# Optimization experiments

Hardware: AMD Instinct MI355X
Metric: run time of the kernel (lower is better)

The kernel has to match this reference:

```python
import jax, jax.numpy as jnp
import numpy as np

B, V = 256, 128000


def setup_inputs() -> dict:
    key = jax.random.key(0)
    k1, k2 = jax.random.split(key)
    logits = jax.random.normal(k1, (B, V), dtype=jnp.float32) * 4.0
    # temperatures in [0.3, 1.2] to avoid division by ~0
    temperatures = jax.random.uniform(k2, (B,), dtype=jnp.float32) * 0.9 + 0.3
    return {"logits": logits, "temperatures": temperatures}


def reference(logits, temperatures):
    # temperature-scaled softmax
    x = logits.astype(jnp.float32) / temperatures[:, None]
    probs = jax.nn.softmax(x, axis=-1)  # (B, V)
    # torch.empty_like(probs).exponential_(1).clamp_min_(1e-10)
    noise = jnp.maximum(
        jax.random.exponential(jax.random.key(42), probs.shape, dtype=jnp.float32),
        1e-10,
    )
    # Gumbel-max style sampling: argmax of probs / Exp(1) noise
    return jnp.argmax(probs / noise, axis=-1)  # (B,) int
```

## Files before the change

### kernel.cpp

```cpp
#include <hip/hip_runtime.h>
#include <stdint.h>
#include <math.h>

#define BB 256
#define ROW 128000
#define SPLIT 16
#define CHUNK (ROW / SPLIT)
#define THREADS 512
#define WAVES (THREADS / 64)
#define EPB (THREADS * 8)
#define GRID (BB * SPLIT)
#define CAP 6144

#define SEED_THREADS 256
#define SEED_STRIDE 496

#define TF_K2 0x1BD11BF0u
#define SMALL_BITS 0x00100000u
#define MIN_L 1.4426950408889634e-10f
#define LN2 0.69314718055994530942f
#define GMAX 33.0f

__device__ __forceinline__ uint32_t rotl32(uint32_t x, int r) {
    return __builtin_amdgcn_alignbit(x, x, 32 - r);
}

#define R1S(r)        { x0 += x1; x1 = rotl32(x1, (r)) ^ x0; }
#define RI1S(r, A, B) { x1 += (B); x0 = x0 + (A) + x1; x1 = rotl32(x1, (r)) ^ x0; }

__device__ __forceinline__ uint32_t threefry1_xor(uint32_t c) {
    uint32_t x1 = c + 42u;
    uint32_t x0 = x1;
    x1 = rotl32(x1, 13) ^ x0;
    R1S(15) R1S(26) R1S(6)
    RI1S(17, 42u, TF_K2 + 1u)
    R1S(29) R1S(16) R1S(24)
    RI1S(13, TF_K2, 2u)
    R1S(15) R1S(26) R1S(6)
    RI1S(17, 0u, 45u)
    R1S(29) R1S(16) R1S(24)
    RI1S(13, 42u, TF_K2 + 4u)
    R1S(15) R1S(26) R1S(6)
    return (x0 + TF_K2) ^ (x1 + 5u);
}

__device__ __forceinline__ void threefry8_xor(uint32_t c, uint32_t bits[8]) {
    uint32_t x0[8], x1[8];
#pragma unroll
    for (int j = 0; j < 8; ++j) x1[j] = c + (uint32_t)(j + 42);
#pragma unroll
    for (int j = 0; j < 8; ++j) { x0[j] = x1[j]; x1[j] = rotl32(x1[j], 13) ^ x0[j]; }

#define RND(r)                                        \
    do { _Pragma("unroll")                            \
        for (int j = 0; j < 8; ++j) {                 \
            x0[j] += x1[j];                           \
            x1[j] = rotl32(x1[j], (r)) ^ x0[j];       \
        } } while (0)
#define RNDI(r, A, B)                                 \
    do { _Pragma("unroll")                            \
        for (int j = 0; j < 8; ++j) {                 \
            x1[j] += (B);                             \
            x0[j] = x0[j] + (A) + x1[j];              \
            x1[j] = rotl32(x1[j], (r)) ^ x0[j];       \
        } } while (0)

    RND(15); RND(26); RND(6);
    RNDI(17, 42u, TF_K2 + 1u);
    RND(29); RND(16); RND(24);
    RNDI(13, TF_K2, 2u);
    RND(15); RND(26); RND(6);
    RNDI(17, 0u, 45u);
    RND(29); RND(16); RND(24);
    RNDI(13, 42u, TF_K2 + 4u);
    RND(15); RND(26); RND(6);
#undef RND
#undef RNDI

#pragma unroll
    for (int j = 0; j < 8; ++j) bits[j] = (x0[j] + TF_K2) ^ (x1[j] + 5u);
}

__device__ __forceinline__ float noise_negL(uint32_t bits) {
    const float uf = __uint_as_float(0x3F800000u | (bits >> 9));
    const float L = __builtin_amdgcn_logf(2.0f - uf);
    const float u = uf - 1.0f;
    const float es2 = u * fmaf(u, fmaf(u, fmaf(u,
        -0.3606737602222408f, -0.4808983469629878f),
        -0.7213475204444817f), -1.4426950408889634f);
    const float es2c = fminf(es2, -MIN_L);
    return (bits < SMALL_BITS) ? es2c : L;
}

__device__ __forceinline__ float score1(float x, float invT2, uint32_t bits) {
    const float L = noise_negL(bits);
    return fmaf(x, invT2, -__builtin_amdgcn_logf(-L));
}

__device__ __forceinline__ uint32_t f2o(float f) {
    uint32_t u = __float_as_uint(f);
    return (u & 0x80000000u) ? ~u : (u | 0x80000000u);
}

__global__ __launch_bounds__(SEED_THREADS) void seed_kernel(
    const float* __restrict__ logits,
    const float* __restrict__ temps,
    float* __restrict__ gs) {
    const int b = blockIdx.x;
    const int t = threadIdx.x;
    const float invT2 = 1.0f / (temps[b] * LN2);
    const int off = t * SEED_STRIDE;
    const float* rowp = logits + (size_t)b * ROW + off;
    const uint32_t cb = (uint32_t)b * ROW + (uint32_t)off;

    const float4 xa = *reinterpret_cast<const float4*>(rowp);
    const float4 xb = *reinterpret_cast<const float4*>(rowp + 4);
    const float xs[8] = {xa.x, xa.y, xa.z, xa.w, xb.x, xb.y, xb.z, xb.w};
    uint32_t bits[8];
    threefry8_xor(cb, bits);

    float bs = -INFINITY;
#pragma unroll
    for (int j = 0; j < 8; ++j) bs = fmaxf(bs, score1(xs[j], invT2, bits[j]));

#pragma unroll
    for (int off2 = 32; off2 >= 1; off2 >>= 1)
        bs = fmaxf(bs, __shfl_xor(bs, off2));

    __shared__ float sred[SEED_THREADS / 64];
    const int lane = t & 63, wid = t >> 6;
    if (lane == 0) sred[wid] = bs;
    __syncthreads();
    if (t == 0)
        gs[b] = fmaxf(fmaxf(sred[0], sred[1]), fmaxf(sred[2], sred[3]));
}

__global__ __launch_bounds__(THREADS, 4) void sampler_kernel(
    const float* __restrict__ logits,
    const float* __restrict__ temps,
    const float* __restrict__ gs,
    unsigned long long* __restrict__ parts) {
    __shared__ int scnt;
    __shared__ unsigned short qidx[CAP];
    __shared__ float qx[CAP];
    __shared__ unsigned long long sbest[WAVES];

    const int g = blockIdx.x;
    const int b = g >> 4;
    const int q = g & 15;
    const float T = temps[b];
    const float invT2 = 1.0f / (T * LN2);
    const float xthr = (gs[b] - GMAX) * (T * LN2);
    const float* rowp = logits + (size_t)b * ROW + (size_t)q * CHUNK;
    const uint32_t cbase = (uint32_t)b * ROW + (uint32_t)(q * CHUNK);
    const int tid = threadIdx.x;
    const int lane = tid & 63;
    const unsigned long long lmask_lt = (1ull << lane) - 1ull;

    if (tid == 0) scnt = 0;
    __syncthreads();

    float xs0[8], xs1[8];
    {
        const int rel = tid * 8;
        const float4 xa = *reinterpret_cast<const float4*>(rowp + rel);
        const float4 xb = *reinterpret_cast<const float4*>(rowp + rel + 4);
        xs0[0]=xa.x; xs0[1]=xa.y; xs0[2]=xa.z; xs0[3]=xa.w;
        xs0[4]=xb.x; xs0[5]=xb.y; xs0[6]=xb.z; xs0[7]=xb.w;
#pragma unroll
        for (int j = 0; j < 8; ++j) {
            const bool pass = xs0[j] > xthr;
            const unsigned long long mk = __ballot(pass);
            if (mk != 0ull) {
                int base = 0;
                if (lane == 0) base = atomicAdd(&scnt, __popcll(mk));
                base = __builtin_amdgcn_readfirstlane(base);
                if (pass) {
                    const int pos = base + (int)__popcll(mk & lmask_lt);
                    if (pos < CAP) {
                        qidx[pos] = (unsigned short)(rel + j);
                        qx[pos] = xs0[j];
                    }
                }
            }
        }
    }
    const int rel1 = EPB + tid * 8;
    const bool in1 = rel1 < CHUNK;
    if (in1) {
        const float4 xa = *reinterpret_cast<const float4*>(rowp + rel1);
        const float4 xb = *reinterpret_cast<const float4*>(rowp + rel1 + 4);
        xs1[0]=xa.x; xs1[1]=xa.y; xs1[2]=xa.z; xs1[3]=xa.w;
        xs1[4]=xb.x; xs1[5]=xb.y; xs1[6]=xb.z; xs1[7]=xb.w;
#pragma unroll
        for (int j = 0; j < 8; ++j) {
            const bool pass = xs1[j] > xthr;
            const unsigned long long mk = __ballot(pass);
            if (mk != 0ull) {
                int base = 0;
                if (lane == 0) base = atomicAdd(&scnt, __popcll(mk));
                base = __builtin_amdgcn_readfirstlane(base);
                if (pass) {
                    const int pos = base + (int)__popcll(mk & lmask_lt);
                    if (pos < CAP) {
                        qidx[pos] = (unsigned short)(rel1 + j);
                        qx[pos] = xs1[j];
                    }
                }
            }
        }
    }
    __syncthreads();

    const int total = scnt;
    float best_s = -INFINITY;
    uint32_t best_rel = 0u;

    if (total > CAP) {
        {
            const int rel = tid * 8;
            uint32_t bits[8];
            threefry8_xor(cbase + (uint32_t)rel, bits);
#pragma unroll
            for (int j = 0; j < 8; ++j) {
                const float s = score1(xs0[j], invT2, bits[j]);
                if (s > best_s) { best_s = s; best_rel = (uint32_t)(rel + j); }
            }
        }
        if (in1) {
            uint32_t bits[8];
            threefry8_xor(cbase + (uint32_t)rel1, bits);
#pragma unroll
            for (int j = 0; j < 8; ++j) {
                const float s = score1(xs1[j], invT2, bits[j]);
                if (s > best_s) { best_s = s; best_rel = (uint32_t)(rel1 + j); }
            }
        }
    } else {
        for (int i = tid; i < total; i += THREADS) {
            const int rel = (int)qidx[i];
            const float x = qx[i];
            const uint32_t bits = threefry1_xor(cbase + (uint32_t)rel);
            const float s = score1(x, invT2, bits);
            if (s > best_s) { best_s = s; best_rel = (uint32_t)rel; }
        }
    }

    const uint32_t best_v = (uint32_t)(q * CHUNK) + best_rel;

    unsigned long long best =
        ((unsigned long long)f2o(best_s) << 32) | (uint32_t)(~best_v);
#pragma unroll
    for (int off = 32; off >= 1; off >>= 1) {
        const unsigned long long o = __shfl_xor(best, off);
        best = (o > best) ? o : best;
    }
    const int wid = tid >> 6;
    if (lane == 0) sbest[wid] = best;
    __syncthreads();
    if (tid == 0) {
        unsigned long long r = sbest[0];
#pragma unroll
        for (int w = 1; w < WAVES; ++w) r = (sbest[w] > r) ? sbest[w] : r;
        parts[g] = r;
    }
}

__global__ __launch_bounds__(BB) void combine_kernel(
    const unsigned long long* __restrict__ parts, int* __restrict__ out) {
    const int b = threadIdx.x;
    const unsigned long long* p = parts + b * SPLIT;
    unsigned long long r = p[0];
#pragma unroll
    for (int w = 1; w < SPLIT; ++w) r = (p[w] > r) ? p[w] : r;
    out[b] = (int)(~(uint32_t)(r & 0xFFFFFFFFull));
}

extern "C" void kernel_launch(void* const* d_in, const int* in_sizes, int n_in,
                              void* d_out, int out_size, void* d_ws, size_t ws_size,
                              hipStream_t stream) {
    const float* logits = (const float*)d_in[0];
    const float* temps = (const float*)d_in[1];
    int* out = (int*)d_out;
    float* gs = (float*)d_ws;
    unsigned long long* parts = (unsigned long long*)((char*)d_ws + 1024);

    hipLaunchKernelGGL(seed_kernel, dim3(BB), dim3(SEED_THREADS), 0, stream,
                       logits, temps, gs);
    hipLaunchKernelGGL(sampler_kernel, dim3(GRID), dim3(THREADS), 0, stream,
                       logits, temps, gs, parts);
    hipLaunchKernelGGL(combine_kernel, dim3(1), dim3(BB), 0, stream, parts, out);
}
```

Measured before the change: 88.48 us.

## Add chunk-max prepass to tighten pruning threshold and pick per-row dense/sparse mode

Adds a chunkmax kernel that reads the whole logits array to find each 4000-element chunk's max logit. The seed kernel folds the noise scores at those maxima into the row bound and counts how many samples pass the threshold, so it can choose a dense or sparse mode per row. The sampler now uses 32 chunks per row and stores only indices in shared memory, re-reading x from global memory. In dense mode it skips the small-value polynomial unless some lane needs it. The cost is one extra full pass over the 131 MB input and an extra kernel launch.

```diff
diff --git a/kernel.cpp b/kernel.cpp
--- a/kernel.cpp
+++ b/kernel.cpp
@@ -4,13 +4,11 @@
 
 #define BB 256
 #define ROW 128000
-#define SPLIT 16
-#define CHUNK (ROW / SPLIT)
+#define SPLITM 32
+#define CHUNKM (ROW / SPLITM)
+#define GRIDM (BB * SPLITM)
 #define THREADS 512
 #define WAVES (THREADS / 64)
-#define EPB (THREADS * 8)
-#define GRID (BB * SPLIT)
-#define CAP 6144
 
 #define SEED_THREADS 256
 #define SEED_STRIDE 496
@@ -20,6 +18,7 @@
 #define MIN_L 1.4426950408889634e-10f
 #define LN2 0.69314718055994530942f
 #define GMAX 33.0f
+#define MODE_CNT_THR 1152
 
 __device__ __forceinline__ uint32_t rotl32(uint32_t x, int r) {
     return __builtin_amdgcn_alignbit(x, x, 32 - r);
@@ -102,13 +101,54 @@
     return (u & 0x80000000u) ? ~u : (u | 0x80000000u);
 }
 
-__global__ __launch_bounds__(SEED_THREADS) void seed_kernel(
-    const float* __restrict__ logits,
-    const float* __restrict__ temps,
-    float* __restrict__ gs) {
+__global__ __launch_bounds__(THREADS) void chunkmax_kernel(
+    const float* __restrict__ logits, float* __restrict__ cmx,
+    uint32_t* __restrict__ cmi) {
+    const int g = blockIdx.x;
+    const int b = g >> 5, q = g & 31;
+    const float* rowp = logits + (size_t)b * ROW + (size_t)q * CHUNKM;
+    const int tid = threadIdx.x;
+    const int rel = tid * 8;
+
+    float mx = -INFINITY;
+    uint32_t mi = 0u;
+    if (rel < CHUNKM) {
+        const float4 xa = *reinterpret_cast<const float4*>(rowp + rel);
+        const float4 xb = *reinterpret_cast<const float4*>(rowp + rel + 4);
+        const float xs[8] = {xa.x, xa.y, xa.z, xa.w, xb.x, xb.y, xb.z, xb.w};
+#pragma unroll
+        for (int j = 0; j < 8; ++j)
+            if (xs[j] > mx) { mx = xs[j]; mi = (uint32_t)(rel + j); }
+    }
+#pragma unroll
+    for (int off = 32; off >= 1; off >>= 1) {
+        const float ox = __shfl_xor(mx, off);
+        const uint32_t oi = __shfl_xor(mi, off);
+        if (ox > mx) { mx = ox; mi = oi; }
+    }
+    __shared__ float smx[WAVES];
+    __shared__ uint32_t smi[WAVES];
+    const int lane = tid & 63, wid = tid >> 6;
+    if (lane == 0) { smx[wid] = mx; smi[wid] = mi; }
+    __syncthreads();
+    if (tid == 0) {
+        mx = smx[0]; mi = smi[0];
+#pragma unroll
+        for (int w = 1; w < WAVES; ++w)
+            if (smx[w] > mx) { mx = smx[w]; mi = smi[w]; }
+        cmx[g] = mx;
+        cmi[g] = (uint32_t)(q * CHUNKM) + mi;
+    }
+}
+
+__global__ __launch_bounds__(SEED_THREADS) void rowseed_kernel(
+    const float* __restrict__ logits, const float* __restrict__ temps,
+    const float* __restrict__ cmx, const uint32_t* __restrict__ cmi,
+    float* __restrict__ gs, int* __restrict__ mode) {
     const int b = blockIdx.x;
     const int t = threadIdx.x;
-    const float invT2 = 1.0f / (temps[b] * LN2);
+    const float T = temps[b];
+    const float invT2 = 1.0f / (T * LN2);
     const int off = t * SEED_STRIDE;
     const float* rowp = logits + (size_t)b * ROW + off;
     const uint32_t cb = (uint32_t)b * ROW + (uint32_t)off;
@@ -123,36 +163,52 @@
 #pragma unroll
     for (int j = 0; j < 8; ++j) bs = fmaxf(bs, score1(xs[j], invT2, bits[j]));
 
-#pragma unroll
-    for (int off2 = 32; off2 >= 1; off2 >>= 1)
-        bs = fmaxf(bs, __shfl_xor(bs, off2));
-
+    if (t < SPLITM) {
+        const uint32_t idx = cmi[b * SPLITM + t];
+        const float xm = cmx[b * SPLITM + t];
+        bs = fmaxf(bs, score1(xm, invT2,
+                              threefry1_xor((uint32_t)b * ROW + idx)));
+    }
+
+#pragma unroll
+    for (int o = 32; o >= 1; o >>= 1) bs = fmaxf(bs, __shfl_xor(bs, o));
     __shared__ float sred[SEED_THREADS / 64];
+    __shared__ int scr[SEED_THREADS / 64];
     const int lane = t & 63, wid = t >> 6;
     if (lane == 0) sred[wid] = bs;
     __syncthreads();
-    if (t == 0)
-        gs[b] = fmaxf(fmaxf(sred[0], sred[1]), fmaxf(sred[2], sred[3]));
+    const float gsv = fmaxf(fmaxf(sred[0], sred[1]), fmaxf(sred[2], sred[3]));
+
+    const float xthr = (gsv - GMAX) * (T * LN2);
+    int c = 0;
+#pragma unroll
+    for (int j = 0; j < 8; ++j) c += (xs[j] > xthr) ? 1 : 0;
+#pragma unroll
+    for (int o = 32; o >= 1; o >>= 1) c += __shfl_xor(c, o);
+    if (lane == 0) scr[wid] = c;
+    __syncthreads();
+    if (t == 0) {
+        const int tot = scr[0] + scr[1] + scr[2] + scr[3];
+        gs[b] = gsv;
+        mode[b] = (tot > MODE_CNT_THR) ? 1 : 0;
+    }
 }
 
 __global__ __launch_bounds__(THREADS, 4) void sampler_kernel(
-    const float* __restrict__ logits,
-    const float* __restrict__ temps,
-    const float* __restrict__ gs,
+    const float* __restrict__ logits, const float* __restrict__ temps,
+    const float* __restrict__ gs, const int* __restrict__ mode,
     unsigned long long* __restrict__ parts) {
     __shared__ int scnt;
-    __shared__ unsigned short qidx[CAP];
-    __shared__ float qx[CAP];
+    __shared__ unsigned short qidx[CHUNKM];
     __shared__ unsigned long long sbest[WAVES];
 
     const int g = blockIdx.x;
-    const int b = g >> 4;
-    const int q = g & 15;
+    const int b = g >> 5, q = g & 31;
     const float T = temps[b];
     const float invT2 = 1.0f / (T * LN2);
     const float xthr = (gs[b] - GMAX) * (T * LN2);
-    const float* rowp = logits + (size_t)b * ROW + (size_t)q * CHUNK;
-    const uint32_t cbase = (uint32_t)b * ROW + (uint32_t)(q * CHUNK);
+    const float* rowp = logits + (size_t)b * ROW + (size_t)q * CHUNKM;
+    const uint32_t cbase = (uint32_t)b * ROW + (uint32_t)(q * CHUNKM);
     const int tid = threadIdx.x;
     const int lane = tid & 63;
     const unsigned long long lmask_lt = (1ull << lane) - 1ull;
@@ -160,94 +216,79 @@
     if (tid == 0) scnt = 0;
     __syncthreads();
 
-    float xs0[8], xs1[8];
-    {
-        const int rel = tid * 8;
+    const int rel = tid * 8;
+    const bool act = rel < CHUNKM;
+    float xs[8];
+    if (act) {
         const float4 xa = *reinterpret_cast<const float4*>(rowp + rel);
         const float4 xb = *reinterpret_cast<const float4*>(rowp + rel + 4);
-        xs0[0]=xa.x; xs0[1]=xa.y; xs0[2]=xa.z; xs0[3]=xa.w;
-        xs0[4]=xb.x; xs0[5]=xb.y; xs0[6]=xb.z; xs0[7]=xb.w;
-#pragma unroll
-        for (int j = 0; j < 8; ++j) {
-            const bool pass = xs0[j] > xthr;
-            const unsigned long long mk = __ballot(pass);
-            if (mk != 0ull) {
-                int base = 0;
-                if (lane == 0) base = atomicAdd(&scnt, __popcll(mk));
-                base = __builtin_amdgcn_readfirstlane(base);
-                if (pass) {
-                    const int pos = base + (int)__popcll(mk & lmask_lt);
-                    if (pos < CAP) {
+        xs[0]=xa.x; xs[1]=xa.y; xs[2]=xa.z; xs[3]=xa.w;
+        xs[4]=xb.x; xs[5]=xb.y; xs[6]=xb.z; xs[7]=xb.w;
+    }
+
+    float best_s = -INFINITY;
+    uint32_t best_rel = 0u;
+
+    if (mode[b]) {
+        if (act) {
+            uint32_t bits[8];
+            threefry8_xor(cbase + (uint32_t)rel, bits);
+            float L8[8];
+#pragma unroll
+            for (int j = 0; j < 8; ++j) {
+                const float uf = __uint_as_float(0x3F800000u | (bits[j] >> 9));
+                L8[j] = __builtin_amdgcn_logf(2.0f - uf);
+            }
+            const uint32_t b01 = min(min(bits[0], bits[1]), bits[2]);
+            const uint32_t b34 = min(min(bits[3], bits[4]), bits[5]);
+            const uint32_t b67 = min(bits[6], bits[7]);
+            if (__any(min(min(b01, b34), b67) < SMALL_BITS)) {
+#pragma unroll
+                for (int j = 0; j < 8; ++j) {
+                    const float u = __uint_as_float(0x3F800000u |
+                                    (bits[j] >> 9)) - 1.0f;
+                    const float es2 = u * fmaf(u, fmaf(u, fmaf(u,
+                        -0.3606737602222408f, -0.4808983469629878f),
+                        -0.7213475204444817f), -1.4426950408889634f);
+                    const float es2c = fminf(es2, -MIN_L);
+                    L8[j] = (bits[j] < SMALL_BITS) ? es2c : L8[j];
+                }
+            }
+#pragma unroll
+            for (int j = 0; j < 8; ++j) {
+                const float s = fmaf(xs[j], invT2,
+                                     -__builtin_amdgcn_logf(-L8[j]));
+                if (s > best_s) { best_s = s; best_rel = (uint32_t)(rel + j); }
+            }
+        }
+    } else {
+        if (act) {
+#pragma unroll
+            for (int j = 0; j < 8; ++j) {
+                const bool pass = xs[j] > xthr;
+                const unsigned long long mk = __ballot(pass);
+                if (mk != 0ull) {
+                    int base = 0;
+                    if (lane == 0) base = atomicAdd(&scnt, __popcll(mk));
+                    base = __builtin_amdgcn_readfirstlane(base);
+                    if (pass) {
+                        const int pos = base + (int)__popcll(mk & lmask_lt);
                         qidx[pos] = (unsigned short)(rel + j);
-                        qx[pos] = xs0[j];
                     }
                 }
             }
         }
-    }
-    const int rel1 = EPB + tid * 8;
-    const bool in1 = rel1 < CHUNK;
-    if (in1) {
-        const float4 xa = *reinterpret_cast<const float4*>(rowp + rel1);
-        const float4 xb = *reinterpret_cast<const float4*>(rowp + rel1 + 4);
-        xs1[0]=xa.x; xs1[1]=xa.y; xs1[2]=xa.z; xs1[3]=xa.w;
-        xs1[4]=xb.x; xs1[5]=xb.y; xs1[6]=xb.z; xs1[7]=xb.w;
-#pragma unroll
-        for (int j = 0; j < 8; ++j) {
-            const bool pass = xs1[j] > xthr;
-            const unsigned long long mk = __ballot(pass);
-            if (mk != 0ull) {
-                int base = 0;
-                if (lane == 0) base = atomicAdd(&scnt, __popcll(mk));
-                base = __builtin_amdgcn_readfirstlane(base);
-                if (pass) {
-                    const int pos = base + (int)__popcll(mk & lmask_lt);
-                    if (pos < CAP) {
-                        qidx[pos] = (unsigned short)(rel1 + j);
-                        qx[pos] = xs1[j];
-                    }
-                }
-            }
+        __syncthreads();
+        const int total = scnt;
+        for (int i = tid; i < total; i += THREADS) {
+            const int r2 = (int)qidx[i];
+            const float x = rowp[r2];
+            const float s = score1(x, invT2, threefry1_xor(cbase + (uint32_t)r2));
+            if (s > best_s) { best_s = s; best_rel = (uint32_t)r2; }
         }
     }
-    __syncthreads();
-
-    const int total = scnt;
-    float best_s = -INFINITY;
-    uint32_t best_rel = 0u;
-
-    if (total > CAP) {
-        {
-            const int rel = tid * 8;
-            uint32_t bits[8];
-            threefry8_xor(cbase + (uint32_t)rel, bits);
-#pragma unroll
-            for (int j = 0; j < 8; ++j) {
-                const float s = score1(xs0[j], invT2, bits[j]);
-                if (s > best_s) { best_s = s; best_rel = (uint32_t)(rel + j); }
-            }
-        }
-        if (in1) {
-            uint32_t bits[8];
-            threefry8_xor(cbase + (uint32_t)rel1, bits);
-#pragma unroll
-            for (int j = 0; j < 8; ++j) {
-                const float s = score1(xs1[j], invT2, bits[j]);
-                if (s > best_s) { best_s = s; best_rel = (uint32_t)(rel1 + j); }
-            }
-        }
-    } else {
-        for (int i = tid; i < total; i += THREADS) {
-            const int rel = (int)qidx[i];
-            const float x = qx[i];
-            const uint32_t bits = threefry1_xor(cbase + (uint32_t)rel);
-            const float s = score1(x, invT2, bits);
-            if (s > best_s) { best_s = s; best_rel = (uint32_t)rel; }
-        }
-    }
-
-    const uint32_t best_v = (uint32_t)(q * CHUNK) + best_rel;
-
+
+    const uint32_t best_v = (uint32_t)(q * CHUNKM) + best_rel;
     unsigned long long best =
         ((unsigned long long)f2o(best_s) << 32) | (uint32_t)(~best_v);
 #pragma unroll
@@ -269,10 +310,10 @@
 __global__ __launch_bounds__(BB) void combine_kernel(
     const unsigned long long* __restrict__ parts, int* __restrict__ out) {
     const int b = threadIdx.x;
-    const unsigned long long* p = parts + b * SPLIT;
+    const unsigned long long* p = parts + b * SPLITM;
     unsigned long long r = p[0];
 #pragma unroll
-    for (int w = 1; w < SPLIT; ++w) r = (p[w] > r) ? p[w] : r;
+    for (int w = 1; w < SPLITM; ++w) r = (p[w] > r) ? p[w] : r;
     out[b] = (int)(~(uint32_t)(r & 0xFFFFFFFFull));
 }
 
@@ -282,12 +323,18 @@
     const float* logits = (const float*)d_in[0];
     const float* temps = (const float*)d_in[1];
     int* out = (int*)d_out;
-    float* gs = (float*)d_ws;
-    unsigned long long* parts = (unsigned long long*)((char*)d_ws + 1024);
-
-    hipLaunchKernelGGL(seed_kernel, dim3(BB), dim3(SEED_THREADS), 0, stream,
-                       logits, temps, gs);
-    hipLaunchKernelGGL(sampler_kernel, dim3(GRID), dim3(THREADS), 0, stream,
-                       logits, temps, gs, parts);
+    float* cmx = (float*)d_ws;
+    uint32_t* cmi = (uint32_t*)((char*)d_ws + 32768);
+    float* gs = (float*)((char*)d_ws + 65536);
+    int* mode = (int*)((char*)d_ws + 66560);
+    unsigned long long* parts =
+        (unsigned long long*)((char*)d_ws + 67584);
+
+    hipLaunchKernelGGL(chunkmax_kernel, dim3(GRIDM), dim3(THREADS), 0, stream,
+                       logits, cmx, cmi);
+    hipLaunchKernelGGL(rowseed_kernel, dim3(BB), dim3(SEED_THREADS), 0, stream,
+                       logits, temps, cmx, cmi, gs, mode);
+    hipLaunchKernelGGL(sampler_kernel, dim3(GRIDM), dim3(THREADS), 0, stream,
+                       logits, temps, gs, mode, parts);
     hipLaunchKernelGGL(combine_kernel, dim3(1), dim3(BB), 0, stream, parts, out);
 }
```

New measurement: 81.13 us. -8.3%, faster.
